# Kernel tuning notes

Measured on AMD Instinct MI355X. Metric: run time of the kernel, lower is better.

## Reference

```python
import jax, jax.numpy as jnp
import numpy as np

N_AGENTS = 2
B, C, H, W = 4, 64, 200, 352


def _conv(x, w, b):
    # x: (n, Cin, H, W), w: (Cout, Cin, 3, 3), 'SAME' padding, stride 1
    y = jax.lax.conv_general_dilated(
        x, w, window_strides=(1, 1), padding='SAME',
        dimension_numbers=('NCHW', 'OIHW', 'NCHW'))
    return y + b[None, :, None, None]


def setup_inputs() -> dict:
    key = jax.random.key(0)
    ks = jax.random.split(key, 4)
    s = 0.05  # small init so sigmoid/tanh stay in useful range
    x = jax.random.normal(ks[0], (N_AGENTS, B, C, H, W), dtype=jnp.float32)
    msg_w = jax.random.normal(ks[1], (C, 2 * C, 3, 3), dtype=jnp.float32) * s
    msg_b = jnp.zeros((C,), jnp.float32)
    gates_w = jax.random.normal(ks[2], (2 * C, 3 * C, 3, 3), dtype=jnp.float32) * s
    gates_b = jnp.zeros((2 * C,), jnp.float32)
    can_w = jax.random.normal(ks[3], (C, 3 * C, 3, 3), dtype=jnp.float32) * s
    can_b = jnp.zeros((C,), jnp.float32)
    return {'x': x, 'msg_w': msg_w, 'msg_b': msg_b,
            'gates_w': gates_w, 'gates_b': gates_b,
            'can_w': can_w, 'can_b': can_b}


def reference(x, msg_w, msg_b, gates_w, gates_b, can_w, can_b):
    # num_iteration=1; only new_x[0] (agent 0's updated feature) is returned,
    # so we compute exactly that path.
    x0, x1 = x[0], x[1]                       # each (B, C, H, W)
    neighbor = jnp.concatenate([x0, x1], axis=1)   # (B, 2C, H, W)
    message = _conv(neighbor, msg_w, msg_b)        # (B, C, H, W)
    agg = 0.5 * (x0 + message)                     # 'avg' over stacked pair
    cat_feat = jnp.concatenate([x0, agg], axis=1)  # (B, 2C, H, W)

    # ConvGRU: batch_first input (1, B, 2C, H, W) -> sequence length B, batch 1
    h0 = jnp.zeros((1, C, H, W), cat_feat.dtype)

    def step(h, inp):
        inp = inp[None]                                     # (1, 2C, H, W)
        comb = jnp.concatenate([inp, h], axis=1)            # (1, 3C, H, W)
        gates = jax.nn.sigmoid(_conv(comb, gates_w, gates_b))
        reset, update = jnp.split(gates, 2, axis=1)         # each (1, C, H, W)
        comb2 = jnp.concatenate([inp, reset * h], axis=1)
        cnm = jnp.tanh(_conv(comb2, can_w, can_b))
        h_next = (1.0 - update) * h + update * cnm
        return h_next, h_next[0]

    _, out = jax.lax.scan(step, h0, cat_feat)  # out: (B, C, H, W)
    return out
```

## Files before the change

kernel.cpp:

```cpp
#include <hip/hip_runtime.h>
#include <math.h>
#include <string.h>

#define HH 200
#define WW 352
#define HWSZ (HH*WW)
#define CHW (64L*HWSZ)

enum { EPI_MSG=0, EPI_GATES=1, EPI_CAND=2 };

typedef __attribute__((ext_vector_type(8))) _Float16 f16x8;
typedef __attribute__((ext_vector_type(4))) float f32x4;
typedef __attribute__((ext_vector_type(4))) unsigned int uint4v;
typedef __attribute__((ext_vector_type(4))) unsigned short ushort4v;

__device__ __forceinline__ unsigned short f2h(float f) {
    _Float16 h = (_Float16)f;
    return __builtin_bit_cast(unsigned short, h);
}
__device__ __forceinline__ float h2f(unsigned short u) {
    return (float)__builtin_bit_cast(_Float16, u);
}

__device__ __forceinline__ void load_lds16(const unsigned short* g,
                                           unsigned short* l) {
    __builtin_amdgcn_global_load_lds(
        (const __attribute__((address_space(1))) unsigned int*)g,
        (__attribute__((address_space(3))) unsigned int*)l, 16, 0, 0);
}

__global__ void prepack_k(const float* __restrict__ mw,
                          const float* __restrict__ gw,
                          const float* __restrict__ cw,
                          unsigned short* __restrict__ pw,
                          unsigned short* __restrict__ zp)
{
    const int MSG_I = 8*9216;
    const int GAT_I = 24*9216;
    const int CAN_I = 12*9216;
    const int TOTAL = MSG_I + GAT_I + CAN_I;
    int idx = blockIdx.x*256 + threadIdx.x;
    if (idx >= TOTAL) {
        int r = idx - TOTAL;
        if (r < 128) zp[r] = 0;
        return;
    }
    const float* w; int cin, nkb, rel; unsigned short* base;
    if (idx < MSG_I)              { w=mw; cin=128; nkb=4; rel=idx;             base=pw; }
    else if (idx < MSG_I+GAT_I)   { w=gw; cin=192; nkb=6; rel=idx-MSG_I;       base=pw+73728; }
    else                          { w=cw; cin=192; nkb=6; rel=idx-MSG_I-GAT_I; base=pw+294912; }
    int chunk = rel / 9216, r = rel - chunk*9216;
    int j = r & 7, lane = (r >> 3) & 63, cfsh = r >> 9;
    int cf = cfsh & 1, sh = cfsh >> 1;
    int q = lane >> 4, n16 = lane & 15;
    int co_l = cf*16 + n16, ch = q*8 + j;
    int cogrp = chunk / nkb, kb = chunk - cogrp*nkb;
    float f = w[(((long)(cogrp*32 + co_l))*cin + kb*32 + ch)*9 + sh];
    base[(size_t)chunk*9216 + r] = f2h(f);
}

__global__ void convert_all_k(const float* __restrict__ x,
                              unsigned short* __restrict__ xb0_all,
                              unsigned short* __restrict__ xb1_all)
{
    int idx = blockIdx.x*256 + threadIdx.x;
    int cp   = idx & 15;
    int rest = idx >> 4;
    int px4  = rest % 17600;
    int r2   = rest / 17600;
    int hb = r2 & 1, ag = (r2 >> 1) & 1, t = r2 >> 2;
    const float* src = x + ((size_t)(ag*4 + t))*CHW
                         + (size_t)(hb*32 + 2*cp)*HWSZ + (size_t)px4*4;
    float4 a = *(const float4*)src;
    float4 b = *(const float4*)(src + HWSZ);
    unsigned int* dst = (unsigned int*)((ag ? xb1_all : xb0_all)
                        + (size_t)t*CHW + (size_t)hb*HWSZ*32) + (size_t)px4*64 + cp;
    dst[0]  = (unsigned)f2h(a.x) | ((unsigned)f2h(b.x) << 16);
    dst[16] = (unsigned)f2h(a.y) | ((unsigned)f2h(b.y) << 16);
    dst[32] = (unsigned)f2h(a.z) | ((unsigned)f2h(b.z) << 16);
    dst[48] = (unsigned)f2h(a.w) | ((unsigned)f2h(b.w) << 16);
}

template<int EPI>
__global__ __launch_bounds__(256, 4)
void conv_mfma_k(const unsigned short* __restrict__ seg0b,
                 const unsigned short* __restrict__ seg1b,
                 const unsigned short* __restrict__ seg2b,
                 int nkb, int nkb_stride, int grp_base,
                 const unsigned short* __restrict__ pw,
                 const unsigned short* __restrict__ zp,
                 const float* __restrict__ bias,
                 const unsigned short* e_hb,
                 const unsigned short* __restrict__ e_updb,
                 float* out_f,
                 unsigned short* out_b,
                 unsigned short* out_b2)
{
    __shared__ unsigned short s_in[340*32];
    __shared__ unsigned short s_w[9*2*64*8];

    const int tid  = threadIdx.x;
    const int lane = tid & 63;
    const int wv   = tid >> 6;
    const int n16  = lane & 15;
    const int q    = lane >> 4;

    int grp, ts = 0;
    if (EPI == EPI_MSG) { ts = blockIdx.z; grp = blockIdx.x & 1; }
    else                { grp = (blockIdx.x & 1) + 2*blockIdx.z + grp_base; }

    const unsigned short* s0 = seg0b + (EPI==EPI_MSG ? (size_t)ts*CHW : 0);
    const unsigned short* s1 = seg1b + (EPI==EPI_MSG ? (size_t)ts*CHW : 0);
    unsigned short* ob = out_b;
    if (EPI == EPI_MSG) ob = (ts < 3) ? out_b + (size_t)ts*CHW : out_b2;

    const int x0p = (blockIdx.x >> 1) * 32;
    const int y0  = blockIdx.y * 8;

    int hdst0 = 0, hdst1 = 0; size_t hsrc0 = 0, hsrc1 = 0;
    bool hval0 = false, hval1 = false;
    {
        auto hcalc = [&](int s, int& hdst, size_t& hsrc, bool& hval) {
            int hp = s >> 2, gs = s & 3;
            int row, col;
            if (hp < 34)      { row = 0; col = hp; }
            else if (hp < 68) { row = 9; col = hp - 34; }
            else { int k = hp - 68; row = 1 + (k >> 1); col = (k & 1) * 33; }
            int pos = row*34 + col;
            int gy = y0 + row - 1, gx = x0p + col - 1;
            hdst = (pos << 5) + (gs << 3);
            int g = (gs ^ pos ^ (pos >> 2)) & 3;
            if ((unsigned)gy < (unsigned)HH && (unsigned)gx < (unsigned)WW) {
                hval = true;
                hsrc = ((size_t)(gy*WW + gx) << 5) + (size_t)(g << 3);
            }
        };
        if (tid < 336) hcalc(tid, hdst0, hsrc0, hval0);
        if (tid < 80)  hcalc(tid + 256, hdst1, hsrc1, hval1);
    }

    auto srcof = [&](int kb) -> const unsigned short* {
        return ((kb < 2) ? s0 : (kb < 4) ? s1 : seg2b) + (size_t)(kb & 1)*HWSZ*32;
    };

    struct HV { uint4v a, b; };
    auto halo_load = [&](int kb, HV& h) {
        const unsigned short* src = srcof(kb);
        if (tid < 336) h.a = *(const uint4v*)(hval0 ? src + hsrc0 : zp);
        if (tid < 80)  h.b = *(const uint4v*)(hval1 ? src + hsrc1 : zp);
    };
    auto halo_write = [&](const HV& h) {
        if (tid < 336) *(uint4v*)&s_in[hdst0] = h.a;
        if (tid < 80)  *(uint4v*)&s_in[hdst1] = h.b;
    };

    auto stage_in = [&](int kb) {
        const unsigned short* src = srcof(kb);
#pragma unroll
        for (int j = 0; j < 4; ++j) {
            const int c    = wv + 4*j;
            const int row  = 1 + (c >> 1);
            const int colh = c & 1;
            const int gy   = y0 + row - 1;
            const int p0   = row*34 + 1 + colh*16;
            const int pl   = p0 + (lane >> 2);
            const int g    = ((lane & 3) ^ pl ^ (pl >> 2)) & 3;
            const int gx   = x0p + colh*16 + (lane >> 2);
            load_lds16(src + (((size_t)(gy*WW + gx)) << 5) + (g << 3),
                       &s_in[(size_t)p0 << 5]);
        }
    };
    auto stage_w = [&](int kb) {
        const unsigned short* wsrc = pw + (size_t)(grp*nkb_stride + kb)*9216;
#pragma unroll
        for (int i = 0; i < 5; ++i) {
            const int u = wv + 4*i;
            if (u < 18)
                load_lds16(wsrc + (size_t)u*512 + (size_t)lane*8, &s_w[(size_t)u*512]);
        }
    };

    f32x4 acc[2][4];
#pragma unroll
    for (int cf=0; cf<2; ++cf)
#pragma unroll
        for (int p=0; p<4; ++p) acc[cf][p] = (f32x4){0.f,0.f,0.f,0.f};

    auto compute = [&]() {
#pragma unroll
        for (int ky = 0; ky < 3; ++ky) {
#pragma unroll
            for (int kx = 0; kx < 3; ++kx) {
                const int sh = ky*3 + kx;
                f16x8 aw0 = *(const f16x8*)&s_w[((sh*2 + 0)*64 + lane)*8];
                f16x8 aw1 = *(const f16x8*)&s_w[((sh*2 + 1)*64 + lane)*8];
#pragma unroll
                for (int p = 0; p < 4; ++p) {
                    const int rl = 2*wv + (p >> 1) + ky;
                    const int cl = 16*(p & 1) + n16 + kx;
                    const int pos = rl*34 + cl;
                    const int sw = (q ^ pos ^ (pos >> 2)) & 3;
                    f16x8 bfr = *(const f16x8*)&s_in[(pos << 5) + (sw << 3)];
                    acc[0][p] = __builtin_amdgcn_mfma_f32_16x16x32_f16(aw0, bfr, acc[0][p], 0, 0, 0);
                    acc[1][p] = __builtin_amdgcn_mfma_f32_16x16x32_f16(aw1, bfr, acc[1][p], 0, 0, 0);
                }
            }
        }
    };

    HV h;
    stage_in(0); stage_w(0); halo_load(0, h);
    halo_write(h);
    __syncthreads();

    for (int kb = 0; kb < nkb; ++kb) {
        if (kb + 1 < nkb) halo_load(kb + 1, h);
        compute();
        __syncthreads();
        if (kb + 1 < nkb) {
            stage_in(kb + 1); stage_w(kb + 1);
            halo_write(h);
            __syncthreads();
        }
    }

#pragma unroll
    for (int cf = 0; cf < 2; ++cf) {
        const int co_r0 = grp*32 + cf*16 + q*4;
        const int half  = (co_r0 >> 5) & 1;
        const int cmod  = co_r0 & 31;
#pragma unroll
        for (int p = 0; p < 4; ++p) {
            const int row = y0 + 2*wv + (p >> 1);
            const int col = x0p + 16*(p & 1) + n16;
            if (row >= HH) continue;
            const long pix = (long)row*WW + col;
            const size_t iidx = (((size_t)half*HWSZ + pix) << 5) + cmod;
            float v[4];
#pragma unroll
            for (int r = 0; r < 4; ++r) v[r] = acc[cf][p][r] + bias[co_r0 + r];

            if (EPI == EPI_MSG) {
                ushort4v xv = *(const ushort4v*)&s0[iidx];
                ushort4v s;
#pragma unroll
                for (int r = 0; r < 4; ++r)
                    s[r] = f2h(0.5f*(h2f(xv[r]) + v[r]));
                *(ushort4v*)&ob[iidx] = s;
            } else if (EPI == EPI_GATES) {
                if (co_r0 < 64) {
                    ushort4v hv = e_hb ? *(const ushort4v*)&e_hb[iidx]
                                       : (ushort4v){0,0,0,0};
                    ushort4v s;
#pragma unroll
                    for (int r = 0; r < 4; ++r) {
                        float g = 1.f/(1.f + __expf(-v[r]));
                        s[r] = f2h(g * h2f(hv[r]));
                    }
                    *(ushort4v*)&out_b[iidx] = s;
                } else {
                    const int cu = co_r0 - 64;
                    const size_t uidx = (((size_t)(cu >> 5)*HWSZ + pix) << 5) + (cu & 31);
                    ushort4v s;
#pragma unroll
                    for (int r = 0; r < 4; ++r)
                        s[r] = f2h(1.f/(1.f + __expf(-v[r])));
                    *(ushort4v*)&out_b2[uidx] = s;
                }
            } else {
                ushort4v uv = *(const ushort4v*)&e_updb[iidx];
                ushort4v hv = e_hb ? *(const ushort4v*)&e_hb[iidx]
                                   : (ushort4v){0,0,0,0};
                ushort4v s;
#pragma unroll
                for (int r = 0; r < 4; ++r) {
                    float cnm = tanhf(v[r]);
                    float u   = h2f(uv[r]);
                    float hn  = (1.f - u)*h2f(hv[r]) + u*cnm;
                    out_f[(long)(co_r0 + r)*HWSZ + pix] = hn;
                    s[r] = f2h(hn);
                }
                *(ushort4v*)&out_b[iidx] = s;
            }
        }
    }
}

extern "C" void kernel_launch(void* const* d_in, const int* in_sizes, int n_in,
                              void* d_out, int out_size, void* d_ws, size_t ws_size,
                              hipStream_t stream)
{
    const float* x       = (const float*)d_in[0];
    const float* msg_w   = (const float*)d_in[1];
    const float* msg_b   = (const float*)d_in[2];
    const float* gates_w = (const float*)d_in[3];
    const float* gates_b = (const float*)d_in[4];
    const float* can_w   = (const float*)d_in[5];
    const float* can_b   = (const float*)d_in[6];
    float* out = (float*)d_out;

    unsigned short* W       = (unsigned short*)d_ws;
    unsigned short* xb0_all = W;
    unsigned short* aggb3   = W + 4*CHW;
    unsigned short* rhb     = W + 5*CHW;
    unsigned short* updb    = W + 6*CHW;
    unsigned short* hb      = W + 7*CHW;
    unsigned short* pw      = W + 8*CHW;
    unsigned short* pw_msg  = pw;
    unsigned short* pw_gat  = pw + 73728;
    unsigned short* pw_can  = pw + 294912;
    unsigned short* zp      = pw + 405504;

    unsigned short* outU16   = (unsigned short*)d_out;
    unsigned short* xb1_all  = outU16;
    unsigned short* aggbase  = outU16 + 4*CHW;

    prepack_k<<<dim3(1585), dim3(256), 0, stream>>>(msg_w, gates_w, can_w, pw, zp);
    convert_all_k<<<dim3(17600), dim3(256), 0, stream>>>(x, xb0_all, xb1_all);

    conv_mfma_k<EPI_MSG><<<dim3(22,25,4), dim3(256), 0, stream>>>(
        xb0_all, xb1_all, nullptr, 4, 4, 0, pw_msg, zp, msg_b,
        nullptr, nullptr, nullptr, aggbase, aggb3);

    for (int t = 0; t < 4; ++t) {
        const unsigned short* xt  = xb0_all + (size_t)t*CHW;
        const unsigned short* agt = (t < 3) ? aggbase + (size_t)t*CHW : aggb3;
        const unsigned short* hprev = t ? hb : nullptr;

        if (t == 0) {
            conv_mfma_k<EPI_GATES><<<dim3(22,25,1), dim3(256), 0, stream>>>(
                xt, agt, nullptr, 4, 6, 2, pw_gat, zp, gates_b,
                nullptr, nullptr, nullptr, rhb, updb);
        } else {
            conv_mfma_k<EPI_GATES><<<dim3(22,25,2), dim3(256), 0, stream>>>(
                xt, agt, hb, 6, 6, 0, pw_gat, zp, gates_b,
                hprev, nullptr, nullptr, rhb, updb);
        }
        conv_mfma_k<EPI_CAND><<<dim3(22,25,1), dim3(256), 0, stream>>>(
            xt, agt, rhb, t ? 6 : 4, 6, 0, pw_can, zp, can_b,
            hprev, updb, out + (size_t)t*CHW, hb, nullptr);
    }
}
```

Baseline: 422.7 us.

## Read conv input fragments directly from global and double-buffer weights in LDS

```diff
diff --git a/kernel.cpp b/kernel.cpp
--- a/kernel.cpp
+++ b/kernel.cpp
@@ -32,19 +32,14 @@
 __global__ void prepack_k(const float* __restrict__ mw,
                           const float* __restrict__ gw,
                           const float* __restrict__ cw,
-                          unsigned short* __restrict__ pw,
-                          unsigned short* __restrict__ zp)
+                          unsigned short* __restrict__ pw)
 {
     const int MSG_I = 8*9216;
     const int GAT_I = 24*9216;
     const int CAN_I = 12*9216;
     const int TOTAL = MSG_I + GAT_I + CAN_I;
     int idx = blockIdx.x*256 + threadIdx.x;
-    if (idx >= TOTAL) {
-        int r = idx - TOTAL;
-        if (r < 128) zp[r] = 0;
-        return;
-    }
+    if (idx >= TOTAL) return;
     const float* w; int cin, nkb, rel; unsigned short* base;
     if (idx < MSG_I)              { w=mw; cin=128; nkb=4; rel=idx;             base=pw; }
     else if (idx < MSG_I+GAT_I)   { w=gw; cin=192; nkb=6; rel=idx-MSG_I;       base=pw+73728; }
@@ -88,7 +83,6 @@
                  const unsigned short* __restrict__ seg2b,
                  int nkb, int nkb_stride, int grp_base,
                  const unsigned short* __restrict__ pw,
-                 const unsigned short* __restrict__ zp,
                  const float* __restrict__ bias,
                  const unsigned short* e_hb,
                  const unsigned short* __restrict__ e_updb,
@@ -96,8 +90,8 @@
                  unsigned short* out_b,
                  unsigned short* out_b2)
 {
-    __shared__ unsigned short s_in[340*32];
-    __shared__ unsigned short s_w[9*2*64*8];
+    __shared__ unsigned short s_w0[9216];
+    __shared__ unsigned short s_w1[9216];
 
     const int tid  = threadIdx.x;
     const int lane = tid & 63;
@@ -116,67 +110,22 @@
 
     const int x0p = (blockIdx.x >> 1) * 32;
     const int y0  = blockIdx.y * 8;
-
-    int hdst0 = 0, hdst1 = 0; size_t hsrc0 = 0, hsrc1 = 0;
-    bool hval0 = false, hval1 = false;
-    {
-        auto hcalc = [&](int s, int& hdst, size_t& hsrc, bool& hval) {
-            int hp = s >> 2, gs = s & 3;
-            int row, col;
-            if (hp < 34)      { row = 0; col = hp; }
-            else if (hp < 68) { row = 9; col = hp - 34; }
-            else { int k = hp - 68; row = 1 + (k >> 1); col = (k & 1) * 33; }
-            int pos = row*34 + col;
-            int gy = y0 + row - 1, gx = x0p + col - 1;
-            hdst = (pos << 5) + (gs << 3);
-            int g = (gs ^ pos ^ (pos >> 2)) & 3;
-            if ((unsigned)gy < (unsigned)HH && (unsigned)gx < (unsigned)WW) {
-                hval = true;
-                hsrc = ((size_t)(gy*WW + gx) << 5) + (size_t)(g << 3);
-            }
-        };
-        if (tid < 336) hcalc(tid, hdst0, hsrc0, hval0);
-        if (tid < 80)  hcalc(tid + 256, hdst1, hsrc1, hval1);
-    }
+    const bool ledge = (x0p == 0);
+    const bool redge = (x0p + 32 == WW);
+
+    const int cb0 = n16*32 + q*8;
+    const int cb1 = (16 + n16)*32 + q*8;
 
     auto srcof = [&](int kb) -> const unsigned short* {
         return ((kb < 2) ? s0 : (kb < 4) ? s1 : seg2b) + (size_t)(kb & 1)*HWSZ*32;
     };
-
-    struct HV { uint4v a, b; };
-    auto halo_load = [&](int kb, HV& h) {
-        const unsigned short* src = srcof(kb);
-        if (tid < 336) h.a = *(const uint4v*)(hval0 ? src + hsrc0 : zp);
-        if (tid < 80)  h.b = *(const uint4v*)(hval1 ? src + hsrc1 : zp);
-    };
-    auto halo_write = [&](const HV& h) {
-        if (tid < 336) *(uint4v*)&s_in[hdst0] = h.a;
-        if (tid < 80)  *(uint4v*)&s_in[hdst1] = h.b;
-    };
-
-    auto stage_in = [&](int kb) {
-        const unsigned short* src = srcof(kb);
-#pragma unroll
-        for (int j = 0; j < 4; ++j) {
-            const int c    = wv + 4*j;
-            const int row  = 1 + (c >> 1);
-            const int colh = c & 1;
-            const int gy   = y0 + row - 1;
-            const int p0   = row*34 + 1 + colh*16;
-            const int pl   = p0 + (lane >> 2);
-            const int g    = ((lane & 3) ^ pl ^ (pl >> 2)) & 3;
-            const int gx   = x0p + colh*16 + (lane >> 2);
-            load_lds16(src + (((size_t)(gy*WW + gx)) << 5) + (g << 3),
-                       &s_in[(size_t)p0 << 5]);
-        }
-    };
-    auto stage_w = [&](int kb) {
+    auto stage_w = [&](int kb, unsigned short* bw) {
         const unsigned short* wsrc = pw + (size_t)(grp*nkb_stride + kb)*9216;
 #pragma unroll
         for (int i = 0; i < 5; ++i) {
             const int u = wv + 4*i;
             if (u < 18)
-                load_lds16(wsrc + (size_t)u*512 + (size_t)lane*8, &s_w[(size_t)u*512]);
+                load_lds16(wsrc + (size_t)u*512 + (size_t)lane*8, &bw[(size_t)u*512]);
         }
     };
 
@@ -186,21 +135,35 @@
 #pragma unroll
         for (int p=0; p<4; ++p) acc[cf][p] = (f32x4){0.f,0.f,0.f,0.f};
 
-    auto compute = [&]() {
+    const f16x8 zfrag = __builtin_bit_cast(f16x8, (uint4v){0u,0u,0u,0u});
+
+    auto compute = [&](int kb, const unsigned short* swt) {
+        const unsigned short* src = srcof(kb);
 #pragma unroll
         for (int ky = 0; ky < 3; ++ky) {
 #pragma unroll
             for (int kx = 0; kx < 3; ++kx) {
                 const int sh = ky*3 + kx;
-                f16x8 aw0 = *(const f16x8*)&s_w[((sh*2 + 0)*64 + lane)*8];
-                f16x8 aw1 = *(const f16x8*)&s_w[((sh*2 + 1)*64 + lane)*8];
+                f16x8 aw0 = *(const f16x8*)&swt[((sh*2 + 0)*64 + lane)*8];
+                f16x8 aw1 = *(const f16x8*)&swt[((sh*2 + 1)*64 + lane)*8];
 #pragma unroll
                 for (int p = 0; p < 4; ++p) {
-                    const int rl = 2*wv + (p >> 1) + ky;
-                    const int cl = 16*(p & 1) + n16 + kx;
-                    const int pos = rl*34 + cl;
-                    const int sw = (q ^ pos ^ (pos >> 2)) & 3;
-                    f16x8 bfr = *(const f16x8*)&s_in[(pos << 5) + (sw << 3)];
+                    const int row = y0 + 2*wv + (p >> 1) + ky - 1;
+                    f16x8 bfr = zfrag;
+                    if ((unsigned)row < (unsigned)HH) {
+                        int off = (row*WW + x0p + kx - 1)*32 + ((p & 1) ? cb1 : cb0);
+                        const bool need_mask = (p & 1) ? (redge && kx == 2)
+                                                       : (ledge && kx == 0);
+                        if (need_mask) {
+                            const int col = x0p + 16*(p & 1) + n16 + kx - 1;
+                            const bool cv = (unsigned)col < (unsigned)WW;
+                            off = off < 0 ? 0 : off;
+                            f16x8 t = *(const f16x8*)(src + off);
+                            bfr = cv ? t : bfr;
+                        } else {
+                            bfr = *(const f16x8*)(src + off);
+                        }
+                    }
                     acc[0][p] = __builtin_amdgcn_mfma_f32_16x16x32_f16(aw0, bfr, acc[0][p], 0, 0, 0);
                     acc[1][p] = __builtin_amdgcn_mfma_f32_16x16x32_f16(aw1, bfr, acc[1][p], 0, 0, 0);
                 }
@@ -208,20 +171,16 @@
         }
     };
 
-    HV h;
-    stage_in(0); stage_w(0); halo_load(0, h);
-    halo_write(h);
-    __syncthreads();
-
-    for (int kb = 0; kb < nkb; ++kb) {
-        if (kb + 1 < nkb) halo_load(kb + 1, h);
-        compute();
+    stage_w(0, s_w0);
+    for (int kb = 0; kb < nkb; kb += 2) {
         __syncthreads();
-        if (kb + 1 < nkb) {
-            stage_in(kb + 1); stage_w(kb + 1);
-            halo_write(h);
-            __syncthreads();
-        }
+        stage_w(kb + 1, s_w1);
+        __builtin_amdgcn_sched_barrier(0);
+        compute(kb, s_w0);
+        __syncthreads();
+        if (kb + 2 < nkb) stage_w(kb + 2, s_w0);
+        __builtin_amdgcn_sched_barrier(0);
+        compute(kb + 1, s_w1);
     }
 
 #pragma unroll
@@ -309,17 +268,16 @@
     unsigned short* pw_msg  = pw;
     unsigned short* pw_gat  = pw + 73728;
     unsigned short* pw_can  = pw + 294912;
-    unsigned short* zp      = pw + 405504;
 
     unsigned short* outU16   = (unsigned short*)d_out;
     unsigned short* xb1_all  = outU16;
     unsigned short* aggbase  = outU16 + 4*CHW;
 
-    prepack_k<<<dim3(1585), dim3(256), 0, stream>>>(msg_w, gates_w, can_w, pw, zp);
+    prepack_k<<<dim3(1584), dim3(256), 0, stream>>>(msg_w, gates_w, can_w, pw);
     convert_all_k<<<dim3(17600), dim3(256), 0, stream>>>(x, xb0_all, xb1_all);
 
     conv_mfma_k<EPI_MSG><<<dim3(22,25,4), dim3(256), 0, stream>>>(
-        xb0_all, xb1_all, nullptr, 4, 4, 0, pw_msg, zp, msg_b,
+        xb0_all, xb1_all, nullptr, 4, 4, 0, pw_msg, msg_b,
         nullptr, nullptr, nullptr, aggbase, aggb3);
 
     for (int t = 0; t < 4; ++t) {
@@ -329,15 +287,15 @@
 
         if (t == 0) {
             conv_mfma_k<EPI_GATES><<<dim3(22,25,1), dim3(256), 0, stream>>>(
-                xt, agt, nullptr, 4, 6, 2, pw_gat, zp, gates_b,
+                xt, agt, nullptr, 4, 6, 2, pw_gat, gates_b,
                 nullptr, nullptr, nullptr, rhb, updb);
         } else {
             conv_mfma_k<EPI_GATES><<<dim3(22,25,2), dim3(256), 0, stream>>>(
-                xt, agt, hb, 6, 6, 0, pw_gat, zp, gates_b,
+                xt, agt, hb, 6, 6, 0, pw_gat, gates_b,
                 hprev, nullptr, nullptr, rhb, updb);
         }
         conv_mfma_k<EPI_CAND><<<dim3(22,25,1), dim3(256), 0, stream>>>(
-            xt, agt, rhb, t ? 6 : 4, 6, 0, pw_can, zp, can_b,
+            xt, agt, rhb, t ? 6 : 4, 6, 0, pw_can, can_b,
             hprev, updb, out + (size_t)t*CHW, hb, nullptr);
     }
 }
```

New measurement: 884.3 us. 2.09x slower.
